# Performance work log

Measured on AMD Instinct MI355X. Metric: run time of the kernel, lower is better.

Reference implementation:

```python
import jax, jax.numpy as jnp
import numpy as np

NUM_HEADS = 16
SQ, B, E = 2048, 4, 1024
SKV = 2049  # 1 text token + SQ motion tokens


def setup_inputs() -> dict:
    key = jax.random.key(0)
    ks = jax.random.split(key, 12)
    s = 1.0 / np.sqrt(E)
    inp = {
        "q": jax.random.normal(ks[0], (SQ, B, E), jnp.float32),
        "kv": jax.random.normal(ks[1], (SKV, B, E), jnp.float32),
        "cond_positions_mask": jax.random.bernoulli(ks[2], 0.3, (B, SQ)),
        "Wq": jax.random.uniform(ks[3], (E, E), jnp.float32, -s, s),
        "bq": jnp.zeros((E,), jnp.float32),
        "Wk": jax.random.uniform(ks[4], (E, E), jnp.float32, -s, s),
        "bk": jnp.zeros((E,), jnp.float32),
        "Wv": jax.random.uniform(ks[5], (E, E), jnp.float32, -s, s),
        "bv": jnp.zeros((E,), jnp.float32),
        "Wo": jax.random.uniform(ks[6], (E, E), jnp.float32, -s, s),
        "bo": jnp.zeros((E,), jnp.float32),
    }
    return inp


def _dual_causal_mask(cond_positions_mask, seq_len_q, seq_len_kv):
    # returns (B, Sq, Skv) bool, True = masked out
    motion_len = seq_len_kv - 1
    i = jnp.arange(seq_len_q)[:, None]
    j = jnp.arange(motion_len)[None, :]
    causal = (i < j)[None]                                  # (1, Sq, ml)
    ci = cond_positions_mask[:, :, None]                    # (B, Sq, 1)
    cj = cond_positions_mask[:, None, :motion_len]          # (B, 1, ml)
    cond_to_cond = ci & cj
    cond_to_gen = ci & ~cj
    motion_mask = (causal & ~cond_to_cond) | cond_to_gen    # (B, Sq, ml)
    b = cond_positions_mask.shape[0]
    text_col = jnp.zeros((b, seq_len_q, 1), bool)           # text token always visible
    return jnp.concatenate([text_col, motion_mask], axis=-1)


def reference(q, kv, cond_positions_mask, Wq, bq, Wk, bk, Wv, bv, Wo, bo):
    seq_len_q, batch, embed_dim = q.shape
    seq_len_kv = kv.shape[0]
    head_dim = embed_dim // NUM_HEADS
    qb = q.transpose(1, 0, 2)   # (B, Sq, E)
    kvb = kv.transpose(1, 0, 2)  # (B, Skv, E)
    Q = (qb @ Wq.T + bq).reshape(batch, seq_len_q, NUM_HEADS, head_dim)
    K = (kvb @ Wk.T + bk).reshape(batch, seq_len_kv, NUM_HEADS, head_dim)
    V = (kvb @ Wv.T + bv).reshape(batch, seq_len_kv, NUM_HEADS, head_dim)
    scores = jnp.einsum("bqhd,bkhd->bhqk", Q, K) / np.sqrt(head_dim).astype(np.float32)
    mask = _dual_causal_mask(cond_positions_mask, seq_len_q, seq_len_kv)
    scores = jnp.where(mask[:, None], -jnp.inf, scores)
    attn = jax.nn.softmax(scores, axis=-1)                  # (B, H, Sq, Skv)
    out = jnp.einsum("bhqk,bkhd->bqhd", attn, V).reshape(batch, seq_len_q, embed_dim)
    out = out @ Wo.T + bo
    return out.transpose(1, 0, 2), attn.mean(axis=1)
```

## Files before the change

### kernel.cpp

```cpp
#include <hip/hip_runtime.h>
#include <hip/hip_bf16.h>

#define B_ 4
#define H_ 16
#define D_ 64
#define E_ 1024
#define SQ_ 2048
#define SKV_ 2049
#define SKVP_ 2080
#define QSCALE 0.18033688011112042f

typedef __attribute__((ext_vector_type(8))) short short8;
typedef __attribute__((ext_vector_type(4))) float f32x4;
typedef __attribute__((ext_vector_type(16))) float f32x16;
typedef __attribute__((ext_vector_type(4))) unsigned int u32x4;
typedef __attribute__((ext_vector_type(4))) float float4v;

static __device__ __forceinline__ float ex2(float x) {
    return __builtin_amdgcn_exp2f(x);
}

static __device__ __forceinline__ unsigned short f2bf(float f) {
    unsigned int u = __float_as_uint(f);
    u += 0x7FFFu + ((u >> 16) & 1u);
    return (unsigned short)(u >> 16);
}
static __device__ __forceinline__ unsigned int pack2(float a, float b) {
    union { __hip_bfloat162 h; unsigned int u; } cv;
    cv.h = __float22bfloat162_rn(make_float2(a, b));
    return cv.u;
}

static __device__ __forceinline__ f32x4 mfma16(short8 a, short8 b, f32x4 c) {
    return __builtin_amdgcn_mfma_f32_16x16x32_bf16(a, b, c, 0, 0, 0);
}
static __device__ __forceinline__ f32x16 mfma32(short8 a, short8 b, f32x16 c) {
    return __builtin_amdgcn_mfma_f32_32x32x16_bf16(a, b, c, 0, 0, 0);
}

__global__ void cvt_bf16_kernel(const float* __restrict__ in,
                                unsigned short* __restrict__ out, int n8) {
    for (int i = blockIdx.x * blockDim.x + threadIdx.x; i < n8; i += gridDim.x * blockDim.x) {
        const float4v a = *(const float4v*)&in[(size_t)i * 8];
        const float4v b = *(const float4v*)&in[(size_t)i * 8 + 4];
        u32x4 o;
        o[0] = pack2(a[0], a[1]);
        o[1] = pack2(a[2], a[3]);
        o[2] = pack2(b[0], b[1]);
        o[3] = pack2(b[2], b[3]);
        *(u32x4*)&out[(size_t)i * 8] = o;
    }
}

__global__ void decode_mask_kernel(const void* __restrict__ mraw,
                                   unsigned char* __restrict__ condm) {
    __shared__ int flags[2];
    const int t = threadIdx.x;
    if (t < 2) flags[t] = 1;
    __syncthreads();
    const unsigned int* wp = (const unsigned int*)mraw;
    int okI = 1, okF = 1;
    for (int i = t; i < 2048; i += 256) {
        unsigned int w = wp[i];
        if (w > 1u) okI = 0;
        if (w != 0u && w != 0x3F800000u) okF = 0;
    }
    if (!okI) atomicAnd(&flags[0], 0);
    if (!okF) atomicAnd(&flags[1], 0);
    __syncthreads();
    const int isWord = flags[0] | flags[1];
    for (int i = t; i < B_ * SQ_; i += 256) {
        unsigned char v;
        if (isWord) v = (unsigned char)(wp[i] != 0u);
        else        v = (unsigned char)(((const unsigned char*)mraw)[i] != 0);
        condm[i] = v;
    }
}

template <int MODE>
__global__ __launch_bounds__(256, 2)
void gemm128_kernel(const unsigned short* __restrict__ Abf,
                    const unsigned short* __restrict__ Wbf,
                    const float* __restrict__ bias, void* __restrict__ Outp,
                    int nrows, int nrb) {
    const int bid = blockIdx.x;
    const int xcd = bid & 7;
    const int pos = bid >> 3;
    const int cb = pos & 7;
    const int rb = (pos >> 3) * 8 + xcd;
    if (rb >= nrb) return;
    const int row0 = rb * 128, col0 = cb * 128;

    __shared__ unsigned short As[128][40];
    __shared__ unsigned short Ws[128][40];
    const int t = threadIdx.x;
    const int w = t >> 6, lane = t & 63;
    const int wm = w >> 1, wn = w & 1;
    const int lr = lane & 15, lg = lane >> 4, lk = lg * 8;
    const int srow = t >> 1, sc0 = (t & 1) * 16;
    int ar = row0 + srow;
    if (ar >= nrows) ar = nrows - 1;
    const int wrow = col0 + srow;

    f32x4 acc[4][4] = {};

#pragma unroll 1
    for (int k0 = 0; k0 < E_; k0 += 32) {
        {
            const unsigned short* ap = &Abf[(size_t)ar * E_ + k0 + sc0];
            *(short8*)&As[srow][sc0] = *(const short8*)&ap[0];
            *(short8*)&As[srow][sc0 + 8] = *(const short8*)&ap[8];
        }
        {
            const unsigned short* wp2 = &Wbf[(size_t)wrow * E_ + k0 + sc0];
            *(short8*)&Ws[srow][sc0] = *(const short8*)&wp2[0];
            *(short8*)&Ws[srow][sc0 + 8] = *(const short8*)&wp2[8];
        }
        __syncthreads();
        short8 af[4], bf[4];
#pragma unroll
        for (int mi = 0; mi < 4; ++mi) af[mi] = *(const short8*)&As[wm * 64 + mi * 16 + lr][lk];
#pragma unroll
        for (int ni = 0; ni < 4; ++ni) bf[ni] = *(const short8*)&Ws[wn * 64 + ni * 16 + lr][lk];
#pragma unroll
        for (int mi = 0; mi < 4; ++mi)
#pragma unroll
            for (int ni = 0; ni < 4; ++ni)
                acc[mi][ni] = mfma16(af[mi], bf[ni], acc[mi][ni]);
        __syncthreads();
    }

#pragma unroll
    for (int ni = 0; ni < 4; ++ni) {
        const int c = col0 + wn * 64 + ni * 16 + lr;
        const float bv = bias[c];
        const int h = c >> 6, d = c & 63;
#pragma unroll
        for (int mi = 0; mi < 4; ++mi) {
#pragma unroll
            for (int r4 = 0; r4 < 4; ++r4) {
                const int r = row0 + wm * 64 + mi * 16 + lg * 4 + r4;
                if (r >= nrows) continue;
                float v = acc[mi][ni][r4] + bv;
                if constexpr (MODE == 0) {
                    v *= QSCALE;
                    const int sq = r >> 2, b = r & 3;
                    ((unsigned short*)Outp)[(((size_t)(b * H_ + h) * SQ_) + sq) * D_ + d] = f2bf(v);
                } else if constexpr (MODE == 1) {
                    const int kvi = r >> 2, b = r & 3;
                    ((unsigned short*)Outp)[(((size_t)(b * H_ + h) * SKVP_) + kvi) * D_ + d] = f2bf(v);
                } else if constexpr (MODE == 2) {
                    const int kvi = r >> 2, b = r & 3;
                    ((unsigned short*)Outp)[(((size_t)(b * H_ + h) * D_) + d) * SKVP_ + kvi] = f2bf(v);
                } else {
                    ((float*)Outp)[(size_t)r * E_ + c] = v;
                }
            }
        }
    }
}

__global__ void zero_pad_kernel(unsigned short* __restrict__ Kb,
                                unsigned short* __restrict__ Vt) {
    const int idx = blockIdx.x * blockDim.x + threadIdx.x;
    const int NK = 64 * 31 * 64;
    if (idx < NK) {
        const int bh = idx / (31 * 64);
        const int rem = idx - bh * 31 * 64;
        const int kvi = SKV_ + rem / 64;
        const int d = rem & 63;
        Kb[((size_t)bh * SKVP_ + kvi) * D_ + d] = 0;
    } else {
        const int j = idx - NK;
        if (j < 4096 * 31) {
            const int row = j / 31;
            const int kvi = SKV_ + (j - row * 31);
            Vt[(size_t)row * SKVP_ + kvi] = 0;
        }
    }
}

__global__ __launch_bounds__(256, 4)
void attn_fwd_kernel(const unsigned short* __restrict__ Qb, const unsigned short* __restrict__ Kb,
                     const unsigned short* __restrict__ Vt, const unsigned char* __restrict__ condm,
                     unsigned short* __restrict__ OP, float* __restrict__ Mst,
                     float* __restrict__ Lst) {
    const int h = blockIdx.y, b = blockIdx.z;
    const int bh = b * H_ + h;
    const int t = threadIdx.x, w = t >> 6, lane = t & 63;
    const int ql = lane & 31;
    const int hi = lane >> 5;
    const int qg = blockIdx.x * 128 + w * 32 + ql;

    __shared__ unsigned short Ks[2 * 64 * 64];
    __shared__ unsigned short Vs[2][64][72];
    __shared__ unsigned int cjb[66];

    for (int g = t; g < 66; g += 256) {
        unsigned int wbits = 0;
        const int base = g * 32;
#pragma unroll 4
        for (int i = 0; i < 32; ++i) {
            const int kv = base + i;
            if (kv >= 1 && kv < SKV_) wbits |= ((unsigned int)condm[b * SQ_ + kv - 1]) << i;
        }
        cjb[g] = wbits;
    }

    const size_t qoff = ((size_t)bh * SQ_ + qg) * D_;
    short8 qf[4];
#pragma unroll
    for (int tt = 0; tt < 4; ++tt) qf[tt] = *(const short8*)&Qb[qoff + tt * 16 + hi * 8];

    const unsigned int ci = condm[b * SQ_ + qg];

    float m = -__builtin_inff(), l = 0.f;
    f32x16 o0 = {}, o1 = {};

    const int krow = t >> 2, kseg2 = (t & 3) * 2;
    const int vrow = t >> 2, vc0 = (t & 3) * 16;
    const unsigned short* Kbase = &Kb[(size_t)bh * SKVP_ * D_];
    const unsigned short* Vbase = &Vt[(size_t)bh * D_ * SKVP_];

    {
        const unsigned short* kp = &Kbase[(size_t)krow * D_];
        const short8 k0 = *(const short8*)&kp[kseg2 * 8];
        const short8 k1 = *(const short8*)&kp[(kseg2 + 1) * 8];
        const unsigned short* vp = &Vbase[(size_t)vrow * SKVP_];
        const short8 v0 = *(const short8*)&vp[vc0];
        const short8 v1 = *(const short8*)&vp[vc0 + 8];
        *(short8*)&Ks[krow * 64 + ((kseg2 ^ (krow & 7)) * 8)] = k0;
        *(short8*)&Ks[krow * 64 + (((kseg2 + 1) ^ (krow & 7)) * 8)] = k1;
        *(short8*)&Vs[0][vrow][vc0] = v0;
        *(short8*)&Vs[0][vrow][vc0 + 8] = v1;
    }
    __syncthreads();

#pragma unroll 1
    for (int it = 0; it < 33; ++it) {
        const int buf = it & 1;
        const int kv0 = it * 64;
        short8 nk0, nk1, nv0, nv1;
        if (it < 32) {
            const int kvn = kv0 + 64;
            int krg = kvn + krow;
            if (krg > SKVP_ - 1) krg = SKVP_ - 1;
            const unsigned short* kp = &Kbase[(size_t)krg * D_];
            nk0 = *(const short8*)&kp[kseg2 * 8];
            nk1 = *(const short8*)&kp[(kseg2 + 1) * 8];
            int vc = kvn + vc0;
            if (vc > SKVP_ - 8) vc = SKVP_ - 8;
            int vc2 = kvn + vc0 + 8;
            if (vc2 > SKVP_ - 8) vc2 = SKVP_ - 8;
            const unsigned short* vp = &Vbase[(size_t)vrow * SKVP_];
            nv0 = *(const short8*)&vp[vc];
            nv1 = *(const short8*)&vp[vc2];
        }

        const unsigned short* Ksb = &Ks[buf * 4096];
#pragma unroll
        for (int ksub = 0; ksub < 2; ++ksub) {
            const int kvg = kv0 + ksub * 32;
            f32x16 S = {};
#pragma unroll
            for (int tt = 0; tt < 4; ++tt) {
                const short8 kf = *(const short8*)&Ksb[(ksub * 32 + ql) * 64 + (((2 * tt + hi) ^ (ql & 7)) * 8)];
                S = mfma32(kf, qf[tt], S);
            }

            const unsigned int cjw = cjb[kvg >> 5];
            const int T = qg + 1 - kvg;
            unsigned int causalw;
            if (T < 0) causalw = ~0u;
            else if (T >= 31) causalw = 0u;
            else causalw = (~0u) << (T + 1);
            unsigned int mb = ci ? ~cjw : causalw;
            if (kvg == 0) mb &= ~1u;
            const unsigned int mbs = mb >> (hi * 4);

#pragma unroll
            for (int r = 0; r < 16; ++r) {
                const int kc = (r & 3) + 8 * (r >> 2);
                S[r] = ((mbs >> kc) & 1u) ? -__builtin_inff() : S[r];
            }
            float t0 = fmaxf(fmaxf(S[0], S[1]), S[2]);
            float t1 = fmaxf(fmaxf(S[3], S[4]), S[5]);
            float t2 = fmaxf(fmaxf(S[6], S[7]), S[8]);
            float t3 = fmaxf(fmaxf(S[9], S[10]), S[11]);
            float t4 = fmaxf(fmaxf(S[12], S[13]), S[14]);
            float rmax = fmaxf(fmaxf(fmaxf(t0, t1), t2), fmaxf(fmaxf(t3, t4), S[15]));
            rmax = fmaxf(rmax, __shfl_xor(rmax, 32));

            if (!__all(rmax <= m + 8.0f)) {
                const float mn = fmaxf(m, rmax);
                const float alpha = ex2(m - mn);
                l *= alpha;
                o0 *= alpha;
                o1 *= alpha;
                m = mn;
            }

#pragma unroll
            for (int r = 0; r < 16; ++r) S[r] = ex2(S[r] - m);
            const float a0s = (S[0] + S[1]) + (S[2] + S[3]);
            const float a1s = (S[4] + S[5]) + (S[6] + S[7]);
            const float a2s = (S[8] + S[9]) + (S[10] + S[11]);
            const float a3s = (S[12] + S[13]) + (S[14] + S[15]);
            float psum = (a0s + a1s) + (a2s + a3s);
            psum += __shfl_xor(psum, 32);
            l += psum;

            const unsigned int w0 = pack2(S[0], S[1]);
            const unsigned int w1 = pack2(S[2], S[3]);
            const unsigned int w2 = pack2(S[4], S[5]);
            const unsigned int w3 = pack2(S[6], S[7]);
            const unsigned int w4 = pack2(S[8], S[9]);
            const unsigned int w5 = pack2(S[10], S[11]);
            const unsigned int w6 = pack2(S[12], S[13]);
            const unsigned int w7 = pack2(S[14], S[15]);
            const unsigned int x0 = __shfl_xor(w0, 32);
            const unsigned int x1 = __shfl_xor(w1, 32);
            const unsigned int x2 = __shfl_xor(w2, 32);
            const unsigned int x3 = __shfl_xor(w3, 32);
            const unsigned int x4 = __shfl_xor(w4, 32);
            const unsigned int x5 = __shfl_xor(w5, 32);
            const unsigned int x6 = __shfl_xor(w6, 32);
            const unsigned int x7 = __shfl_xor(w7, 32);
            union { u32x4 u; short8 s8; } pb0, pb1;
            pb0.u = (u32x4){hi ? x2 : w0, hi ? x3 : w1, hi ? w2 : x0, hi ? w3 : x1};
            pb1.u = (u32x4){hi ? x6 : w4, hi ? x7 : w5, hi ? w6 : x4, hi ? w7 : x5};

            const short8 vf00 = *(const short8*)&Vs[buf][ql][ksub * 32 + hi * 8];
            const short8 vf01 = *(const short8*)&Vs[buf][ql][ksub * 32 + 16 + hi * 8];
            const short8 vf10 = *(const short8*)&Vs[buf][32 + ql][ksub * 32 + hi * 8];
            const short8 vf11 = *(const short8*)&Vs[buf][32 + ql][ksub * 32 + 16 + hi * 8];
            o0 = mfma32(vf00, pb0.s8, o0);
            o0 = mfma32(vf01, pb1.s8, o0);
            o1 = mfma32(vf10, pb0.s8, o1);
            o1 = mfma32(vf11, pb1.s8, o1);
        }

        if (it < 32) {
            const int nb = (buf ^ 1) * 4096;
            *(short8*)&Ks[nb + krow * 64 + ((kseg2 ^ (krow & 7)) * 8)] = nk0;
            *(short8*)&Ks[nb + krow * 64 + (((kseg2 + 1) ^ (krow & 7)) * 8)] = nk1;
            *(short8*)&Vs[buf ^ 1][vrow][vc0] = nv0;
            *(short8*)&Vs[buf ^ 1][vrow][vc0 + 8] = nv1;
        }
        __syncthreads();
    }

    const float linv = 1.0f / l;
    unsigned short* opbase = &OP[((size_t)qg * B_ + b) * E_ + h * D_];
#pragma unroll
    for (int rp = 0; rp < 8; ++rp) {
        const int r0 = rp * 2, r1 = r0 + 1;
        const int d = ((r0 & 3) + 8 * (r0 >> 2)) + 4 * hi;
        *(unsigned int*)(opbase + d) = pack2(o0[r0] * linv, o0[r1] * linv);
        *(unsigned int*)(opbase + 32 + d) = pack2(o1[r0] * linv, o1[r1] * linv);
    }
    if (hi == 0) {
        Mst[(size_t)bh * SQ_ + qg] = m;
        Lst[(size_t)bh * SQ_ + qg] = linv;
    }
}

__global__ __launch_bounds__(256, 4)
void attn_probs_kernel(const unsigned short* __restrict__ Qb, const unsigned short* __restrict__ Kb,
                       const float* __restrict__ Mst, const float* __restrict__ Linv,
                       const unsigned char* __restrict__ condm, float* __restrict__ out1) {
    const int bid = blockIdx.x;
    const int xcd = bid & 7;
    const int pos = bid >> 3;
    const int qi = pos & 3;
    const int rest = pos >> 2;
    const int kvb = rest % 33;
    const int b = rest / 33;
    const int qblk = xcd * 4 + qi;
    const int kv0 = kvb * 64;

    const int t = threadIdx.x, w = t >> 6, lane = t & 63;
    const int ql = lane & 31, hi = lane >> 5;
    const int kc = w >> 1, qc = w & 1;
    const int qg = qblk * 64 + qc * 32 + ql;

    __shared__ char smem[17408];
    unsigned short* Ks = (unsigned short*)smem;
    float* Tr = (float*)smem;
    __shared__ unsigned int cjw2[2];

    if (t < 64) {
        const int kvv = kv0 + t;
        int pred = 0;
        if (kvv >= 1 && kvv < SKV_) pred = condm[b * SQ_ + kvv - 1];
        const unsigned long long bal = __ballot(pred != 0);
        if (t == 0) { cjw2[0] = (unsigned int)bal; cjw2[1] = (unsigned int)(bal >> 32); }
    }
    const unsigned int ci = condm[b * SQ_ + qg];

    const int krow = t >> 2;
    const int kseg2 = (t & 3) * 2;
    int ksrc = kv0 + krow;
    if (ksrc >= SKVP_) ksrc = SKVP_ - 1;

    {
        const unsigned short* kp = &Kb[((size_t)(b * H_) * SKVP_ + ksrc) * D_];
        const short8 k0 = *(const short8*)&kp[kseg2 * 8];
        const short8 k1 = *(const short8*)&kp[(kseg2 + 1) * 8];
        *(short8*)&Ks[krow * 64 + ((kseg2 ^ (krow & 7)) * 8)] = k0;
        *(short8*)&Ks[krow * 64 + (((kseg2 + 1) ^ (krow & 7)) * 8)] = k1;
    }
    __syncthreads();

    const int kvg = kv0 + kc * 32;
    unsigned int mb;
    {
        const unsigned int cjw = cjw2[kc];
        const int T = qg + 1 - kvg;
        unsigned int causalw;
        if (T < 0) causalw = ~0u;
        else if (T >= 31) causalw = 0u;
        else causalw = (~0u) << (T + 1);
        mb = ci ? ~cjw : causalw;
        if (kvg == 0) mb &= ~1u;
    }
    const unsigned int mbs = mb >> (hi * 4);

    float acc[16] = {};

#pragma unroll 1
    for (int h = 0; h < H_; ++h) {
        const int buf = h & 1;
        const int bh = b * H_ + h;
        short8 nk0, nk1;
        if (h < H_ - 1) {
            const unsigned short* kp = &Kb[((size_t)(bh + 1) * SKVP_ + ksrc) * D_];
            nk0 = *(const short8*)&kp[kseg2 * 8];
            nk1 = *(const short8*)&kp[(kseg2 + 1) * 8];
        }

        const size_t qoff = ((size_t)bh * SQ_ + qg) * D_;
        short8 qf[4];
#pragma unroll
        for (int tt = 0; tt < 4; ++tt) qf[tt] = *(const short8*)&Qb[qoff + tt * 16 + hi * 8];
        const float mh = Mst[(size_t)bh * SQ_ + qg];
        const float li = Linv[(size_t)bh * SQ_ + qg] * (1.0f / 16.0f);

        const unsigned short* Ksb = &Ks[buf * 4096];
        f32x16 S = {};
#pragma unroll
        for (int tt = 0; tt < 4; ++tt) {
            const short8 kf = *(const short8*)&Ksb[(kc * 32 + ql) * 64 + (((2 * tt + hi) ^ (ql & 7)) * 8)];
            S = mfma32(kf, qf[tt], S);
        }
#pragma unroll
        for (int r = 0; r < 16; ++r) {
            const int kk = (r & 3) + 8 * (r >> 2);
            const float p = ((mbs >> kk) & 1u) ? 0.f : ex2(S[r] - mh);
            acc[r] += p * li;
        }

        if (h < H_ - 1) {
            const int nb = (buf ^ 1) * 4096;
            *(short8*)&Ks[nb + krow * 64 + ((kseg2 ^ (krow & 7)) * 8)] = nk0;
            *(short8*)&Ks[nb + krow * 64 + (((kseg2 + 1) ^ (krow & 7)) * 8)] = nk1;
        }
        __syncthreads();
    }

    float* Trw = &Tr[w * (32 * 33)];
#pragma unroll
    for (int r = 0; r < 16; ++r) {
        const int kk = (r & 3) + 8 * (r >> 2) + 4 * hi;
        Trw[ql * 33 + kk] = acc[r];
    }
    const int kcol = kv0 + kc * 32 + ql;
    const int qb_w = qblk * 64 + qc * 32;
    if (kcol < SKV_) {
#pragma unroll
        for (int step = 0; step < 16; ++step) {
            const int q2 = step * 2 + hi;
            out1[((size_t)b * SQ_ + qb_w + q2) * SKV_ + kcol] = Trw[q2 * 33 + ql];
        }
    }
}

extern "C" void kernel_launch(void* const* d_in, const int* in_sizes, int n_in,
                              void* d_out, int out_size, void* d_ws, size_t ws_size,
                              hipStream_t stream) {
    const float* q   = (const float*)d_in[0];
    const float* kv  = (const float*)d_in[1];
    const void*  msk = d_in[2];
    const float* Wq  = (const float*)d_in[3];
    const float* bq  = (const float*)d_in[4];
    const float* Wk  = (const float*)d_in[5];
    const float* bk  = (const float*)d_in[6];
    const float* Wv  = (const float*)d_in[7];
    const float* bv  = (const float*)d_in[8];
    const float* Wo  = (const float*)d_in[9];
    const float* bo  = (const float*)d_in[10];

    char* ws = (char*)d_ws;
    unsigned short* qbf = (unsigned short*)(ws);
    unsigned short* OP  = (unsigned short*)(ws);
    unsigned short* kvbf= (unsigned short*)(ws + 16777216);
    unsigned short* Wqb = (unsigned short*)(ws + 33562624);
    unsigned short* Wkb = (unsigned short*)(ws + 35659776);
    unsigned short* Wvb = (unsigned short*)(ws + 37756928);
    unsigned short* Wob = (unsigned short*)(ws + 39854080);
    unsigned short* Qb  = (unsigned short*)(ws + 41951232);
    unsigned short* Kb  = (unsigned short*)(ws + 58728448);
    unsigned short* Vt  = (unsigned short*)(ws + 75767808);
    float*          Mst = (float*)(ws + 92807168);
    float*          Lst = (float*)(ws + 93331456);
    unsigned char* condm = (unsigned char*)(ws + 93855744);

    float* out0 = (float*)d_out;
    float* out1 = out0 + (size_t)SQ_ * B_ * E_;

    decode_mask_kernel<<<1, 256, 0, stream>>>(msk, condm);
    cvt_bf16_kernel<<<2048, 256, 0, stream>>>(q, qbf, (SQ_ * B_ * E_) / 8);
    cvt_bf16_kernel<<<2048, 256, 0, stream>>>(kv, kvbf, (SKV_ * B_ * E_) / 8);
    cvt_bf16_kernel<<<512, 256, 0, stream>>>(Wq, Wqb, (E_ * E_) / 8);
    cvt_bf16_kernel<<<512, 256, 0, stream>>>(Wk, Wkb, (E_ * E_) / 8);
    cvt_bf16_kernel<<<512, 256, 0, stream>>>(Wv, Wvb, (E_ * E_) / 8);
    cvt_bf16_kernel<<<512, 256, 0, stream>>>(Wo, Wob, (E_ * E_) / 8);
    gemm128_kernel<0><<<512, 256, 0, stream>>>(qbf, Wqb, bq, (void*)Qb, SQ_ * B_, 64);
    gemm128_kernel<1><<<576, 256, 0, stream>>>(kvbf, Wkb, bk, (void*)Kb, SKV_ * B_, 65);
    gemm128_kernel<2><<<576, 256, 0, stream>>>(kvbf, Wvb, bv, (void*)Vt, SKV_ * B_, 65);
    zero_pad_kernel<<<992, 256, 0, stream>>>(Kb, Vt);
    attn_fwd_kernel<<<dim3(16, 16, 4), 256, 0, stream>>>(Qb, Kb, Vt, condm, OP, Mst, Lst);
    attn_probs_kernel<<<4224, 256, 0, stream>>>(Qb, Kb, Mst, Lst, condm, out1);
    gemm128_kernel<3><<<512, 256, 0, stream>>>(OP, Wob, bo, (void*)out0, SQ_ * B_, 64);
}
```

Before: 511.0 us.

## Use direct global-to-LDS loads in GEMM, fold softmax normalizer, prefetch Q in probs

The projection GEMM moves to 512 threads with 8 waves, each computing a 64x32 sub-tile. It loads A and W tiles with global_load_lds straight into unpadded LDS, skipping the register round trip. The attention forward kernel now stores a single combined log-normalizer (max + log2(sum) + log2(16)), so the probs kernel computes exp2(S - m') directly without a separate 1/l multiply and 1/16 scale. The probs kernel's head loop is unrolled by two with a fixed ping-pong K buffer, and Q and stats for the next head are prefetched during the current head's compute. The unpadded LDS layout may cause bank conflicts on fragment reads, and using log2 of l could slightly change precision.

```diff
diff --git a/kernel.cpp b/kernel.cpp
--- a/kernel.cpp
+++ b/kernel.cpp
@@ -36,6 +36,12 @@
 }
 static __device__ __forceinline__ f32x16 mfma32(short8 a, short8 b, f32x16 c) {
     return __builtin_amdgcn_mfma_f32_32x32x16_bf16(a, b, c, 0, 0, 0);
+}
+
+static __device__ __forceinline__ void gload16(const void* g, void* l) {
+    __builtin_amdgcn_global_load_lds(
+        (const __attribute__((address_space(1))) unsigned int*)g,
+        (__attribute__((address_space(3))) unsigned int*)l, 16, 0, 0);
 }
 
 __global__ void cvt_bf16_kernel(const float* __restrict__ in,
@@ -78,7 +84,7 @@
 }
 
 template <int MODE>
-__global__ __launch_bounds__(256, 2)
+__global__ __launch_bounds__(512, 2)
 void gemm128_kernel(const unsigned short* __restrict__ Abf,
                     const unsigned short* __restrict__ Wbf,
                     const float* __restrict__ bias, void* __restrict__ Outp,
@@ -91,48 +97,48 @@
     if (rb >= nrb) return;
     const int row0 = rb * 128, col0 = cb * 128;
 
-    __shared__ unsigned short As[128][40];
-    __shared__ unsigned short Ws[128][40];
+    __shared__ unsigned short As[128 * 32];
+    __shared__ unsigned short Ws[128 * 32];
     const int t = threadIdx.x;
     const int w = t >> 6, lane = t & 63;
-    const int wm = w >> 1, wn = w & 1;
+    const int wm = w >> 2, wn = w & 3;
     const int lr = lane & 15, lg = lane >> 4, lk = lg * 8;
-    const int srow = t >> 1, sc0 = (t & 1) * 16;
+
+    const int srow = w * 16 + (lane >> 2);
+    const int scol = (lane & 3) * 8;
     int ar = row0 + srow;
     if (ar >= nrows) ar = nrows - 1;
     const int wrow = col0 + srow;
-
-    f32x4 acc[4][4] = {};
+    const unsigned short* agp = &Abf[(size_t)ar * E_ + scol];
+    const unsigned short* wgp = &Wbf[(size_t)wrow * E_ + scol];
+    unsigned short* lAs = &As[(size_t)w * 512 + (size_t)lane * 8];
+    unsigned short* lWs = &Ws[(size_t)w * 512 + (size_t)lane * 8];
+
+    f32x4 acc[4][2] = {};
 
 #pragma unroll 1
     for (int k0 = 0; k0 < E_; k0 += 32) {
-        {
-            const unsigned short* ap = &Abf[(size_t)ar * E_ + k0 + sc0];
-            *(short8*)&As[srow][sc0] = *(const short8*)&ap[0];
-            *(short8*)&As[srow][sc0 + 8] = *(const short8*)&ap[8];
-        }
-        {
-            const unsigned short* wp2 = &Wbf[(size_t)wrow * E_ + k0 + sc0];
-            *(short8*)&Ws[srow][sc0] = *(const short8*)&wp2[0];
-            *(short8*)&Ws[srow][sc0 + 8] = *(const short8*)&wp2[8];
-        }
+        gload16(agp + k0, lAs);
+        gload16(wgp + k0, lWs);
         __syncthreads();
-        short8 af[4], bf[4];
-#pragma unroll
-        for (int mi = 0; mi < 4; ++mi) af[mi] = *(const short8*)&As[wm * 64 + mi * 16 + lr][lk];
-#pragma unroll
-        for (int ni = 0; ni < 4; ++ni) bf[ni] = *(const short8*)&Ws[wn * 64 + ni * 16 + lr][lk];
+        short8 af[4], bf2[2];
 #pragma unroll
         for (int mi = 0; mi < 4; ++mi)
-#pragma unroll
-            for (int ni = 0; ni < 4; ++ni)
-                acc[mi][ni] = mfma16(af[mi], bf[ni], acc[mi][ni]);
+            af[mi] = *(const short8*)&As[(wm * 64 + mi * 16 + lr) * 32 + lk];
+#pragma unroll
+        for (int ni = 0; ni < 2; ++ni)
+            bf2[ni] = *(const short8*)&Ws[(wn * 32 + ni * 16 + lr) * 32 + lk];
+#pragma unroll
+        for (int mi = 0; mi < 4; ++mi)
+#pragma unroll
+            for (int ni = 0; ni < 2; ++ni)
+                acc[mi][ni] = mfma16(af[mi], bf2[ni], acc[mi][ni]);
         __syncthreads();
     }
 
 #pragma unroll
-    for (int ni = 0; ni < 4; ++ni) {
-        const int c = col0 + wn * 64 + ni * 16 + lr;
+    for (int ni = 0; ni < 2; ++ni) {
+        const int c = col0 + wn * 32 + ni * 16 + lr;
         const float bv = bias[c];
         const int h = c >> 6, d = c & 63;
 #pragma unroll
@@ -183,8 +189,7 @@
 __global__ __launch_bounds__(256, 4)
 void attn_fwd_kernel(const unsigned short* __restrict__ Qb, const unsigned short* __restrict__ Kb,
                      const unsigned short* __restrict__ Vt, const unsigned char* __restrict__ condm,
-                     unsigned short* __restrict__ OP, float* __restrict__ Mst,
-                     float* __restrict__ Lst) {
+                     unsigned short* __restrict__ OP, float* __restrict__ Mst) {
     const int h = blockIdx.y, b = blockIdx.z;
     const int bh = b * H_ + h;
     const int t = threadIdx.x, w = t >> 6, lane = t & 63;
@@ -360,14 +365,13 @@
         *(unsigned int*)(opbase + 32 + d) = pack2(o1[r0] * linv, o1[r1] * linv);
     }
     if (hi == 0) {
-        Mst[(size_t)bh * SQ_ + qg] = m;
-        Lst[(size_t)bh * SQ_ + qg] = linv;
+        Mst[(size_t)bh * SQ_ + qg] = m + __log2f(l) + 4.0f;
     }
 }
 
 __global__ __launch_bounds__(256, 4)
 void attn_probs_kernel(const unsigned short* __restrict__ Qb, const unsigned short* __restrict__ Kb,
-                       const float* __restrict__ Mst, const float* __restrict__ Linv,
+                       const float* __restrict__ Mstp,
                        const unsigned char* __restrict__ condm, float* __restrict__ out1) {
     const int bid = blockIdx.x;
     const int xcd = bid & 7;
@@ -409,6 +413,14 @@
         const short8 k1 = *(const short8*)&kp[(kseg2 + 1) * 8];
         *(short8*)&Ks[krow * 64 + ((kseg2 ^ (krow & 7)) * 8)] = k0;
         *(short8*)&Ks[krow * 64 + (((kseg2 + 1) ^ (krow & 7)) * 8)] = k1;
+    }
+    short8 qfA[4], qfB[4];
+    float mpA, mpB;
+    {
+        const size_t qoff = ((size_t)(b * H_) * SQ_ + qg) * D_;
+#pragma unroll
+        for (int tt = 0; tt < 4; ++tt) qfA[tt] = *(const short8*)&Qb[qoff + tt * 16 + hi * 8];
+        mpA = Mstp[(size_t)(b * H_) * SQ_ + qg];
     }
     __syncthreads();
 
@@ -429,43 +441,66 @@
     float acc[16] = {};
 
 #pragma unroll 1
-    for (int h = 0; h < H_; ++h) {
-        const int buf = h & 1;
-        const int bh = b * H_ + h;
-        short8 nk0, nk1;
-        if (h < H_ - 1) {
-            const unsigned short* kp = &Kb[((size_t)(bh + 1) * SKVP_ + ksrc) * D_];
-            nk0 = *(const short8*)&kp[kseg2 * 8];
-            nk1 = *(const short8*)&kp[(kseg2 + 1) * 8];
-        }
-
-        const size_t qoff = ((size_t)bh * SQ_ + qg) * D_;
-        short8 qf[4];
-#pragma unroll
-        for (int tt = 0; tt < 4; ++tt) qf[tt] = *(const short8*)&Qb[qoff + tt * 16 + hi * 8];
-        const float mh = Mst[(size_t)bh * SQ_ + qg];
-        const float li = Linv[(size_t)bh * SQ_ + qg] * (1.0f / 16.0f);
-
-        const unsigned short* Ksb = &Ks[buf * 4096];
-        f32x16 S = {};
-#pragma unroll
-        for (int tt = 0; tt < 4; ++tt) {
-            const short8 kf = *(const short8*)&Ksb[(kc * 32 + ql) * 64 + (((2 * tt + hi) ^ (ql & 7)) * 8)];
-            S = mfma32(kf, qf[tt], S);
-        }
-#pragma unroll
-        for (int r = 0; r < 16; ++r) {
-            const int kk = (r & 3) + 8 * (r >> 2);
-            const float p = ((mbs >> kk) & 1u) ? 0.f : ex2(S[r] - mh);
-            acc[r] += p * li;
-        }
-
-        if (h < H_ - 1) {
-            const int nb = (buf ^ 1) * 4096;
-            *(short8*)&Ks[nb + krow * 64 + ((kseg2 ^ (krow & 7)) * 8)] = nk0;
-            *(short8*)&Ks[nb + krow * 64 + (((kseg2 + 1) ^ (krow & 7)) * 8)] = nk1;
-        }
-        __syncthreads();
+    for (int hp = 0; hp < 8; ++hp) {
+        {
+            const int bh1 = b * H_ + 2 * hp + 1;
+            short8 nk0, nk1;
+            {
+                const unsigned short* kp = &Kb[((size_t)bh1 * SKVP_ + ksrc) * D_];
+                nk0 = *(const short8*)&kp[kseg2 * 8];
+                nk1 = *(const short8*)&kp[(kseg2 + 1) * 8];
+            }
+            {
+                const size_t qoff = ((size_t)bh1 * SQ_ + qg) * D_;
+#pragma unroll
+                for (int tt = 0; tt < 4; ++tt) qfB[tt] = *(const short8*)&Qb[qoff + tt * 16 + hi * 8];
+                mpB = Mstp[(size_t)bh1 * SQ_ + qg];
+            }
+            f32x16 S = {};
+#pragma unroll
+            for (int tt = 0; tt < 4; ++tt) {
+                const short8 kf = *(const short8*)&Ks[(kc * 32 + ql) * 64 + (((2 * tt + hi) ^ (ql & 7)) * 8)];
+                S = mfma32(kf, qfA[tt], S);
+            }
+#pragma unroll
+            for (int r = 0; r < 16; ++r) {
+                const int kk = (r & 3) + 8 * (r >> 2);
+                acc[r] += ((mbs >> kk) & 1u) ? 0.f : ex2(S[r] - mpA);
+            }
+            *(short8*)&Ks[4096 + krow * 64 + ((kseg2 ^ (krow & 7)) * 8)] = nk0;
+            *(short8*)&Ks[4096 + krow * 64 + (((kseg2 + 1) ^ (krow & 7)) * 8)] = nk1;
+            __syncthreads();
+        }
+        {
+            short8 nk0, nk1;
+            const bool more = (hp < 7);
+            if (more) {
+                const int bh2 = b * H_ + 2 * hp + 2;
+                const unsigned short* kp = &Kb[((size_t)bh2 * SKVP_ + ksrc) * D_];
+                nk0 = *(const short8*)&kp[kseg2 * 8];
+                nk1 = *(const short8*)&kp[(kseg2 + 1) * 8];
+                const size_t qoff = ((size_t)bh2 * SQ_ + qg) * D_;
+#pragma unroll
+                for (int tt = 0; tt < 4; ++tt) qfA[tt] = *(const short8*)&Qb[qoff + tt * 16 + hi * 8];
+                mpA = Mstp[(size_t)bh2 * SQ_ + qg];
+            }
+            f32x16 S = {};
+#pragma unroll
+            for (int tt = 0; tt < 4; ++tt) {
+                const short8 kf = *(const short8*)&Ks[4096 + (kc * 32 + ql) * 64 + (((2 * tt + hi) ^ (ql & 7)) * 8)];
+                S = mfma32(kf, qfB[tt], S);
+            }
+#pragma unroll
+            for (int r = 0; r < 16; ++r) {
+                const int kk = (r & 3) + 8 * (r >> 2);
+                acc[r] += ((mbs >> kk) & 1u) ? 0.f : ex2(S[r] - mpB);
+            }
+            if (more) {
+                *(short8*)&Ks[krow * 64 + ((kseg2 ^ (krow & 7)) * 8)] = nk0;
+                *(short8*)&Ks[krow * 64 + (((kseg2 + 1) ^ (krow & 7)) * 8)] = nk1;
+            }
+            __syncthreads();
+        }
     }
 
     float* Trw = &Tr[w * (32 * 33)];
@@ -512,7 +547,6 @@
     unsigned short* Kb  = (unsigned short*)(ws + 58728448);
     unsigned short* Vt  = (unsigned short*)(ws + 75767808);
     float*          Mst = (float*)(ws + 92807168);
-    float*          Lst = (float*)(ws + 93331456);
     unsigned char* condm = (unsigned char*)(ws + 93855744);
 
     float* out0 = (float*)d_out;
@@ -525,11 +559,11 @@
     cvt_bf16_kernel<<<512, 256, 0, stream>>>(Wk, Wkb, (E_ * E_) / 8);
     cvt_bf16_kernel<<<512, 256, 0, stream>>>(Wv, Wvb, (E_ * E_) / 8);
     cvt_bf16_kernel<<<512, 256, 0, stream>>>(Wo, Wob, (E_ * E_) / 8);
-    gemm128_kernel<0><<<512, 256, 0, stream>>>(qbf, Wqb, bq, (void*)Qb, SQ_ * B_, 64);
-    gemm128_kernel<1><<<576, 256, 0, stream>>>(kvbf, Wkb, bk, (void*)Kb, SKV_ * B_, 65);
-    gemm128_kernel<2><<<576, 256, 0, stream>>>(kvbf, Wvb, bv, (void*)Vt, SKV_ * B_, 65);
+    gemm128_kernel<0><<<512, 512, 0, stream>>>(qbf, Wqb, bq, (void*)Qb, SQ_ * B_, 64);
+    gemm128_kernel<1><<<576, 512, 0, stream>>>(kvbf, Wkb, bk, (void*)Kb, SKV_ * B_, 65);
+    gemm128_kernel<2><<<576, 512, 0, stream>>>(kvbf, Wvb, bv, (void*)Vt, SKV_ * B_, 65);
     zero_pad_kernel<<<992, 256, 0, stream>>>(Kb, Vt);
-    attn_fwd_kernel<<<dim3(16, 16, 4), 256, 0, stream>>>(Qb, Kb, Vt, condm, OP, Mst, Lst);
-    attn_probs_kernel<<<4224, 256, 0, stream>>>(Qb, Kb, Mst, Lst, condm, out1);
-    gemm128_kernel<3><<<512, 256, 0, stream>>>(OP, Wob, bo, (void*)out0, SQ_ * B_, 64);
-}
+    attn_fwd_kernel<<<dim3(16, 16, 4), 256, 0, stream>>>(Qb, Kb, Vt, condm, OP, Mst);
+    attn_probs_kernel<<<4224, 256, 0, stream>>>(Qb, Kb, Mst, condm, out1);
+    gemm128_kernel<3><<<512, 512, 0, stream>>>(OP, Wob, bo, (void*)out0, SQ_ * B_, 64);
+}
```

Result: faster. 453.6 us (-11.2%).
